# Performance work log

Hardware: AMD Instinct MI355X
Metric: run time of the kernel (lower is better)

## Reference

```python
import jax, jax.numpy as jnp
import numpy as np

NUM_EXPERTS = 8
TOP_K = 2
HIDDEN = 1024
INTER_TOTAL = 8192  # intermediate_size * experts_per_rank
B, S = 2, 2048


def setup_inputs() -> dict:
    key = jax.random.key(0)
    k1, k2, k3, k4, k5, k6 = jax.random.split(key, 6)
    T = B * S
    x = jax.random.normal(k1, (B, S, HIDDEN), dtype=jnp.float32)
    scores = jax.random.uniform(k2, (T, NUM_EXPERTS), dtype=jnp.float32)
    expert_weights = jax.random.uniform(k3, (T, TOP_K), dtype=jnp.float32)
    top_experts = jax.random.randint(k4, (T, TOP_K), 0, NUM_EXPERTS, dtype=jnp.int32)
    w1 = jax.random.normal(k5, (HIDDEN, INTER_TOTAL), dtype=jnp.float32) * 0.02
    w2 = jax.random.normal(k6, (INTER_TOTAL, HIDDEN), dtype=jnp.float32) * 0.02
    return {"x": x, "scores": scores, "expert_weights": expert_weights,
            "top_experts": top_experts, "w1": w1, "w2": w2}


def reference(x, scores, expert_weights, top_experts, w1, w2):
    # forward_once with expert_parallel_size == 1 (dropless MoE dispatch/combine).
    in_shape = x.shape
    T = in_shape[0] * in_shape[1]
    H = in_shape[-1]
    x_flat = x.reshape(T, H)

    flat_experts = top_experts.reshape(-1)          # [T*top_k]
    flat_weights = expert_weights.reshape(-1)       # [T*top_k]

    # ops.sort: stable radix sort of routed copies by expert id
    order = jnp.argsort(flat_experts, stable=True)  # "indices"
    token_idx = order // TOP_K                      # source token per sorted slot

    # padded_gather: bucket tokens per expert (padding rows are zeros and
    # pass through the bias-free MLP as zeros, so they never affect output)
    xg = x_flat[token_idx]                          # [T*top_k, H]

    # MLP: w1 -> gelu(tanh approx) -> w2
    h = jax.nn.gelu(xg @ w1, approximate=True)      # [T*top_k, inter*E]
    y = h @ w2                                      # [T*top_k, H]

    # padded_scatter: weighted combine back to token order
    w_sorted = flat_weights[order]
    out = jnp.zeros((T, H), dtype=x.dtype).at[token_idx].add(w_sorted[:, None] * y)
    return out.reshape(in_shape)
```

## Files before the change

### kernel.cpp

```cpp
#include <hip/hip_runtime.h>
#include <hip/hip_bf16.h>
#include <math.h>

#define HID 1024
#define INTER 8192
#define TT 4096

typedef __bf16 bf16x8 __attribute__((ext_vector_type(8)));
typedef float f32x4 __attribute__((ext_vector_type(4)));

__device__ __forceinline__ void gll16(const void* g, void* l) {
    __builtin_amdgcn_global_load_lds(
        (const __attribute__((address_space(1))) void*)g,
        (__attribute__((address_space(3))) void*)l, 16, 0, 0);
}

template <int OFF>
__device__ __forceinline__ bf16x8 ds_read128o(unsigned addr) {
    bf16x8 r;
    asm volatile("ds_read_b128 %0, %1 offset:%c2" : "=v"(r) : "v"(addr), "i"(OFF));
    return r;
}

__global__ void k_prep(const float* __restrict__ x, const float* __restrict__ ew,
                       __hip_bfloat16* __restrict__ xb, float* __restrict__ s,
                       int n4, int T) {
    int stride = gridDim.x * blockDim.x;
    for (int i = blockIdx.x * blockDim.x + threadIdx.x; i < n4; i += stride) {
        float4 v = ((const float4*)x)[i];
        __hip_bfloat16* o = xb + (size_t)i * 4;
        o[0] = __float2bfloat16(v.x);
        o[1] = __float2bfloat16(v.y);
        o[2] = __float2bfloat16(v.z);
        o[3] = __float2bfloat16(v.w);
    }
    for (int t = blockIdx.x * blockDim.x + threadIdx.x; t < T; t += stride)
        s[t] = ew[2 * t] + ew[2 * t + 1];
}

__global__ void k_tcast(const float* __restrict__ in, __hip_bfloat16* __restrict__ out,
                        int R, int C) {
    __shared__ float tile[32][33];
    const int tx = threadIdx.x & 31, ty = threadIdx.x >> 5;
    const int br = blockIdx.y * 32, bc = blockIdx.x * 32;
#pragma unroll
    for (int j = 0; j < 32; j += 8)
        tile[ty + j][tx] = in[(size_t)(br + ty + j) * C + bc + tx];
    __syncthreads();
#pragma unroll
    for (int j = 0; j < 32; j += 8)
        out[(size_t)(bc + ty + j) * R + br + tx] = __float2bfloat16(tile[tx][ty + j]);
}

template <int EPI>
__global__ __launch_bounds__(256, 2) void k_g128(
    const __hip_bfloat16* __restrict__ A, const __hip_bfloat16* __restrict__ Bt,
    __hip_bfloat16* __restrict__ hOut, float* __restrict__ fOut,
    const float* __restrict__ s, int Kfull, int nt, int Nout) {
    __shared__ __hip_bfloat16 sA[2][128][64];
    __shared__ __hip_bfloat16 sB[2][128][64];
    const int tid = threadIdx.x;
    const int lane = tid & 63, wid = tid >> 6;
    const int wr = wid >> 1, wc = wid & 1;

    const int nwg = gridDim.x * gridDim.y;
    const int wg = blockIdx.y * gridDim.x + blockIdx.x;
    const int swz = (wg & 7) * (nwg >> 3) + (wg >> 3);
    const int brow = (swz / gridDim.x) * 128;
    const int bcol = (swz % gridDim.x) * 128;
    const size_t kbase = (size_t)blockIdx.z * ((size_t)nt * 64);

    const int colsw = (((lane & 7) ^ (lane >> 3)) << 3);
    const __hip_bfloat16* gA2 =
        A + (size_t)(brow + wid * 32 + (lane >> 3)) * Kfull + kbase + colsw;
    const __hip_bfloat16* gB2 =
        Bt + (size_t)(bcol + wid * 32 + (lane >> 3)) * Kfull + kbase + colsw;
    char* ldsA2 = (char*)&sA[0][0][0] + wid * 4096;
    char* ldsB2 = (char*)&sB[0][0][0] + wid * 4096;
    const size_t chunkStep = (size_t)8 * Kfull;

    const unsigned baseA = (unsigned)(uintptr_t)&sA[0][0][0];
    const unsigned baseB = (unsigned)(uintptr_t)&sB[0][0][0];
    const unsigned g0 = (((lane >> 4)) ^ (lane & 7)) << 4;
    const unsigned g1 = ((4 + (lane >> 4)) ^ (lane & 7)) << 4;
    const unsigned rdA0 = baseA + wr * 8192 + (lane & 15) * 128 + g0;
    const unsigned rdA1 = baseA + wr * 8192 + (lane & 15) * 128 + g1;
    const unsigned rdB0 = baseB + wc * 8192 + (lane & 15) * 128 + g0;
    const unsigned rdB1 = baseB + wc * 8192 + (lane & 15) * 128 + g1;

    f32x4 acc[4][4] = {};
    bf16x8 aF[4][2], b01[2][2], b23[2][2];

#define STAGE_AB(bufoff, t)                                                    \
    do {                                                                       \
        _Pragma("unroll") for (int j = 0; j < 4; ++j)                          \
            gll16(gA2 + (size_t)j * chunkStep + (size_t)(t) * 64,              \
                  ldsA2 + (bufoff) + j * 1024);                                \
        _Pragma("unroll") for (int j = 0; j < 4; ++j)                          \
            gll16(gB2 + (size_t)j * chunkStep + (size_t)(t) * 64,              \
                  ldsB2 + (bufoff) + j * 1024);                                \
    } while (0)
#define PIN() __builtin_amdgcn_sched_barrier(0)
#define BAR()                              \
    do {                                   \
        PIN();                             \
        __builtin_amdgcn_s_barrier();      \
        PIN();                             \
    } while (0)
#define WAIT_LG4() __builtin_amdgcn_s_waitcnt(0xC47F)
#define WAIT_LG0() __builtin_amdgcn_s_waitcnt(0xC07F)
#define WAIT_VM0() __builtin_amdgcn_s_waitcnt(0x0F70)

    STAGE_AB(0u, 0);
    WAIT_VM0();
    BAR();

#pragma unroll 1
    for (int i = 0; i < nt; ++i) {
        const unsigned co = (i & 1) ? 16384u : 0u;
        const unsigned no = co ^ 16384u;
        const bool full = (i + 1 < nt);
        const unsigned aA0 = rdA0 + co, aA1 = rdA1 + co;
        const unsigned aB0 = rdB0 + co, aB1 = rdB1 + co;

        aF[0][0] = ds_read128o<0>(aA0);
        aF[0][1] = ds_read128o<0>(aA1);
        aF[1][0] = ds_read128o<2048>(aA0);
        aF[1][1] = ds_read128o<2048>(aA1);
        aF[2][0] = ds_read128o<4096>(aA0);
        aF[2][1] = ds_read128o<4096>(aA1);
        aF[3][0] = ds_read128o<6144>(aA0);
        aF[3][1] = ds_read128o<6144>(aA1);
        b01[0][0] = ds_read128o<0>(aB0);
        b01[0][1] = ds_read128o<0>(aB1);
        b01[1][0] = ds_read128o<2048>(aB0);
        b01[1][1] = ds_read128o<2048>(aB1);
        b23[0][0] = ds_read128o<4096>(aB0);
        b23[0][1] = ds_read128o<4096>(aB1);
        b23[1][0] = ds_read128o<6144>(aB0);
        b23[1][1] = ds_read128o<6144>(aB1);

        if (full) STAGE_AB(no, i + 1);

        __builtin_amdgcn_s_setprio(1);
        WAIT_LG4();
        PIN();
#pragma unroll
        for (int ks = 0; ks < 2; ++ks)
#pragma unroll
            for (int m = 0; m < 4; ++m)
#pragma unroll
                for (int n = 0; n < 2; ++n)
                    acc[m][n] = __builtin_amdgcn_mfma_f32_16x16x32_bf16(
                        aF[m][ks], b01[n][ks], acc[m][n], 0, 0, 0);
        PIN();
        WAIT_LG0();
        PIN();
#pragma unroll
        for (int ks = 0; ks < 2; ++ks)
#pragma unroll
            for (int m = 0; m < 4; ++m)
#pragma unroll
                for (int n = 0; n < 2; ++n)
                    acc[m][2 + n] = __builtin_amdgcn_mfma_f32_16x16x32_bf16(
                        aF[m][ks], b23[n][ks], acc[m][2 + n], 0, 0, 0);
        __builtin_amdgcn_s_setprio(0);
        PIN();
        WAIT_VM0();
        BAR();
    }

    const int orow = brow + wr * 64 + ((lane >> 4) << 2);
    const int ocol = bcol + wc * 64 + (lane & 15);
#pragma unroll
    for (int m = 0; m < 4; ++m) {
#pragma unroll
        for (int j = 0; j < 4; ++j) {
            const int r = orow + m * 16 + j;
            const size_t ro = (size_t)r * Nout;
            if (EPI == 0) {
#pragma unroll
                for (int n = 0; n < 4; ++n) {
                    float v = acc[m][n][j];
                    float u = 1.5957691216057308f * (v + 0.044715f * v * v * v);
                    float g = v / (1.0f + __expf(-u));
                    hOut[ro + ocol + n * 16] = __float2bfloat16(g);
                }
            } else {
                const float sc = s[r];
#pragma unroll
                for (int n = 0; n < 4; ++n)
                    unsafeAtomicAdd(&fOut[ro + ocol + n * 16], sc * acc[m][n][j]);
            }
        }
    }
#undef STAGE_AB
#undef PIN
#undef BAR
#undef WAIT_LG4
#undef WAIT_LG0
#undef WAIT_VM0
}

extern "C" void kernel_launch(void* const* d_in, const int* in_sizes, int n_in,
                              void* d_out, int out_size, void* d_ws, size_t ws_size,
                              hipStream_t stream) {
    const float* x = (const float*)d_in[0];
    const float* ew = (const float*)d_in[2];
    const float* w1 = (const float*)d_in[4];
    const float* w2 = (const float*)d_in[5];
    float* out = (float*)d_out;

    char* ws = (char*)d_ws;
    float* s = (float*)ws;
    __hip_bfloat16* xb = (__hip_bfloat16*)(ws + 16384);
    __hip_bfloat16* w1t = (__hip_bfloat16*)(ws + 16384 + 8388608);
    __hip_bfloat16* w2t = (__hip_bfloat16*)(ws + 16384 + 8388608 + 16777216);
    __hip_bfloat16* h = (__hip_bfloat16*)(ws + 16384 + 8388608 + 2 * 16777216);

    k_prep<<<1024, 256, 0, stream>>>(x, ew, xb, s, (TT * HID) / 4, TT);

    dim3 t1(INTER / 32, HID / 32);
    k_tcast<<<t1, 256, 0, stream>>>(w1, w1t, HID, INTER);
    dim3 t2(HID / 32, INTER / 32);
    k_tcast<<<t2, 256, 0, stream>>>(w2, w2t, INTER, HID);

    dim3 g1(INTER / 128, TT / 128, 1);
    k_g128<0><<<g1, 256, 0, stream>>>(xb, w1t, h, nullptr, nullptr, HID, HID / 64, INTER);

    hipMemsetAsync(out, 0, (size_t)TT * HID * sizeof(float), stream);
    dim3 g2(HID / 128, TT / 128, 4);
    k_g128<1><<<g2, 256, 0, stream>>>(h, w2t, nullptr, out, s, INTER, 2048 / 64, HID);
}
```

Baseline: 226.4 us.

## Switch GEMM to triple-buffered K=32 tiles with two-stage prefetch

Both GEMMs now use a K-tile of 32 instead of 64 and three LDS buffers instead of two. Loads are issued two iterations ahead, and each iteration waits only for the older tile. LDS use drops from 64KB to 48KB, and launch bounds rise to 3 blocks per CU to allow more occupancy. The cost is twice as many barriers per K step and half as many MFMAs per barrier, and the new swizzle and pointer layout must still be correct.

```diff
diff --git a/kernel.cpp b/kernel.cpp
--- a/kernel.cpp
+++ b/kernel.cpp
@@ -53,12 +53,12 @@
 }
 
 template <int EPI>
-__global__ __launch_bounds__(256, 2) void k_g128(
+__global__ __launch_bounds__(256, 3) void k_g3(
     const __hip_bfloat16* __restrict__ A, const __hip_bfloat16* __restrict__ Bt,
     __hip_bfloat16* __restrict__ hOut, float* __restrict__ fOut,
     const float* __restrict__ s, int Kfull, int nt, int Nout) {
-    __shared__ __hip_bfloat16 sA[2][128][64];
-    __shared__ __hip_bfloat16 sB[2][128][64];
+    __shared__ __hip_bfloat16 sA[3][128][32];
+    __shared__ __hip_bfloat16 sB[3][128][32];
     const int tid = threadIdx.x;
     const int lane = tid & 63, wid = tid >> 6;
     const int wr = wid >> 1, wc = wid & 1;
@@ -68,37 +68,32 @@
     const int swz = (wg & 7) * (nwg >> 3) + (wg >> 3);
     const int brow = (swz / gridDim.x) * 128;
     const int bcol = (swz % gridDim.x) * 128;
-    const size_t kbase = (size_t)blockIdx.z * ((size_t)nt * 64);
-
-    const int colsw = (((lane & 7) ^ (lane >> 3)) << 3);
+    const size_t kbase = (size_t)blockIdx.z * ((size_t)nt * 32);
+
+    const int colsw = (((lane & 3) ^ ((lane >> 2) & 3)) << 3);
     const __hip_bfloat16* gA2 =
-        A + (size_t)(brow + wid * 32 + (lane >> 3)) * Kfull + kbase + colsw;
+        A + (size_t)(brow + wid * 32 + (lane >> 2)) * Kfull + kbase + colsw;
     const __hip_bfloat16* gB2 =
-        Bt + (size_t)(bcol + wid * 32 + (lane >> 3)) * Kfull + kbase + colsw;
-    char* ldsA2 = (char*)&sA[0][0][0] + wid * 4096;
-    char* ldsB2 = (char*)&sB[0][0][0] + wid * 4096;
-    const size_t chunkStep = (size_t)8 * Kfull;
+        Bt + (size_t)(bcol + wid * 32 + (lane >> 2)) * Kfull + kbase + colsw;
+    char* ldsA2 = (char*)&sA[0][0][0] + wid * 2048;
+    char* ldsB2 = (char*)&sB[0][0][0] + wid * 2048;
+    const size_t chunkStep = (size_t)16 * Kfull;
 
     const unsigned baseA = (unsigned)(uintptr_t)&sA[0][0][0];
     const unsigned baseB = (unsigned)(uintptr_t)&sB[0][0][0];
-    const unsigned g0 = (((lane >> 4)) ^ (lane & 7)) << 4;
-    const unsigned g1 = ((4 + (lane >> 4)) ^ (lane & 7)) << 4;
-    const unsigned rdA0 = baseA + wr * 8192 + (lane & 15) * 128 + g0;
-    const unsigned rdA1 = baseA + wr * 8192 + (lane & 15) * 128 + g1;
-    const unsigned rdB0 = baseB + wc * 8192 + (lane & 15) * 128 + g0;
-    const unsigned rdB1 = baseB + wc * 8192 + (lane & 15) * 128 + g1;
+    const unsigned gsw = (((lane >> 4) ^ (lane & 3)) << 4);
+    const unsigned rdA = baseA + wr * 4096 + (lane & 15) * 64 + gsw;
+    const unsigned rdB = baseB + wc * 4096 + (lane & 15) * 64 + gsw;
 
     f32x4 acc[4][4] = {};
-    bf16x8 aF[4][2], b01[2][2], b23[2][2];
-
-#define STAGE_AB(bufoff, t)                                                    \
+    bf16x8 aF[4], bF[4];
+
+#define STAGE(bufoff, t)                                                       \
     do {                                                                       \
-        _Pragma("unroll") for (int j = 0; j < 4; ++j)                          \
-            gll16(gA2 + (size_t)j * chunkStep + (size_t)(t) * 64,              \
-                  ldsA2 + (bufoff) + j * 1024);                                \
-        _Pragma("unroll") for (int j = 0; j < 4; ++j)                          \
-            gll16(gB2 + (size_t)j * chunkStep + (size_t)(t) * 64,              \
-                  ldsB2 + (bufoff) + j * 1024);                                \
+        gll16(gA2 + (size_t)(t) * 32, ldsA2 + (bufoff));                       \
+        gll16(gA2 + chunkStep + (size_t)(t) * 32, ldsA2 + (bufoff) + 1024);    \
+        gll16(gB2 + (size_t)(t) * 32, ldsB2 + (bufoff));                       \
+        gll16(gB2 + chunkStep + (size_t)(t) * 32, ldsB2 + (bufoff) + 1024);    \
     } while (0)
 #define PIN() __builtin_amdgcn_sched_barrier(0)
 #define BAR()                              \
@@ -107,67 +102,62 @@
         __builtin_amdgcn_s_barrier();      \
         PIN();                             \
     } while (0)
-#define WAIT_LG4() __builtin_amdgcn_s_waitcnt(0xC47F)
+#define WAIT_LG2() __builtin_amdgcn_s_waitcnt(0xC27F)
 #define WAIT_LG0() __builtin_amdgcn_s_waitcnt(0xC07F)
+#define WAIT_VM4() __builtin_amdgcn_s_waitcnt(0x0F74)
 #define WAIT_VM0() __builtin_amdgcn_s_waitcnt(0x0F70)
 
-    STAGE_AB(0u, 0);
-    WAIT_VM0();
+    STAGE(0u, 0);
+    STAGE(8192u, 1);
+    WAIT_VM4();
     BAR();
 
+    unsigned co = 0u, c1 = 8192u, c2 = 16384u;
 #pragma unroll 1
     for (int i = 0; i < nt; ++i) {
-        const unsigned co = (i & 1) ? 16384u : 0u;
-        const unsigned no = co ^ 16384u;
-        const bool full = (i + 1 < nt);
-        const unsigned aA0 = rdA0 + co, aA1 = rdA1 + co;
-        const unsigned aB0 = rdB0 + co, aB1 = rdB1 + co;
-
-        aF[0][0] = ds_read128o<0>(aA0);
-        aF[0][1] = ds_read128o<0>(aA1);
-        aF[1][0] = ds_read128o<2048>(aA0);
-        aF[1][1] = ds_read128o<2048>(aA1);
-        aF[2][0] = ds_read128o<4096>(aA0);
-        aF[2][1] = ds_read128o<4096>(aA1);
-        aF[3][0] = ds_read128o<6144>(aA0);
-        aF[3][1] = ds_read128o<6144>(aA1);
-        b01[0][0] = ds_read128o<0>(aB0);
-        b01[0][1] = ds_read128o<0>(aB1);
-        b01[1][0] = ds_read128o<2048>(aB0);
-        b01[1][1] = ds_read128o<2048>(aB1);
-        b23[0][0] = ds_read128o<4096>(aB0);
-        b23[0][1] = ds_read128o<4096>(aB1);
-        b23[1][0] = ds_read128o<6144>(aB0);
-        b23[1][1] = ds_read128o<6144>(aB1);
-
-        if (full) STAGE_AB(no, i + 1);
+        const bool more = (i + 2 < nt);
+        const unsigned aA = rdA + co, aB = rdB + co;
+
+        aF[0] = ds_read128o<0>(aA);
+        aF[1] = ds_read128o<1024>(aA);
+        aF[2] = ds_read128o<2048>(aA);
+        aF[3] = ds_read128o<3072>(aA);
+        bF[0] = ds_read128o<0>(aB);
+        bF[1] = ds_read128o<1024>(aB);
+        bF[2] = ds_read128o<2048>(aB);
+        bF[3] = ds_read128o<3072>(aB);
+
+        if (more) STAGE(c2, i + 2);
 
         __builtin_amdgcn_s_setprio(1);
-        WAIT_LG4();
-        PIN();
-#pragma unroll
-        for (int ks = 0; ks < 2; ++ks)
-#pragma unroll
-            for (int m = 0; m < 4; ++m)
-#pragma unroll
-                for (int n = 0; n < 2; ++n)
-                    acc[m][n] = __builtin_amdgcn_mfma_f32_16x16x32_bf16(
-                        aF[m][ks], b01[n][ks], acc[m][n], 0, 0, 0);
+        WAIT_LG2();
+        PIN();
+#pragma unroll
+        for (int m = 0; m < 4; ++m)
+#pragma unroll
+            for (int n = 0; n < 2; ++n)
+                acc[m][n] = __builtin_amdgcn_mfma_f32_16x16x32_bf16(
+                    aF[m], bF[n], acc[m][n], 0, 0, 0);
         PIN();
         WAIT_LG0();
         PIN();
 #pragma unroll
-        for (int ks = 0; ks < 2; ++ks)
-#pragma unroll
-            for (int m = 0; m < 4; ++m)
-#pragma unroll
-                for (int n = 0; n < 2; ++n)
-                    acc[m][2 + n] = __builtin_amdgcn_mfma_f32_16x16x32_bf16(
-                        aF[m][ks], b23[n][ks], acc[m][2 + n], 0, 0, 0);
+        for (int m = 0; m < 4; ++m)
+#pragma unroll
+            for (int n = 0; n < 2; ++n)
+                acc[m][2 + n] = __builtin_amdgcn_mfma_f32_16x16x32_bf16(
+                    aF[m], bF[2 + n], acc[m][2 + n], 0, 0, 0);
         __builtin_amdgcn_s_setprio(0);
         PIN();
-        WAIT_VM0();
+        if (more)
+            WAIT_VM4();
+        else
+            WAIT_VM0();
         BAR();
+        const unsigned t = co;
+        co = c1;
+        c1 = c2;
+        c2 = t;
     }
 
     const int orow = brow + wr * 64 + ((lane >> 4) << 2);
@@ -194,11 +184,12 @@
             }
         }
     }
-#undef STAGE_AB
+#undef STAGE
 #undef PIN
 #undef BAR
-#undef WAIT_LG4
+#undef WAIT_LG2
 #undef WAIT_LG0
+#undef WAIT_VM4
 #undef WAIT_VM0
 }
 
@@ -226,9 +217,9 @@
     k_tcast<<<t2, 256, 0, stream>>>(w2, w2t, INTER, HID);
 
     dim3 g1(INTER / 128, TT / 128, 1);
-    k_g128<0><<<g1, 256, 0, stream>>>(xb, w1t, h, nullptr, nullptr, HID, HID / 64, INTER);
+    k_g3<0><<<g1, 256, 0, stream>>>(xb, w1t, h, nullptr, nullptr, HID, HID / 32, INTER);
 
     hipMemsetAsync(out, 0, (size_t)TT * HID * sizeof(float), stream);
     dim3 g2(HID / 128, TT / 128, 4);
-    k_g128<1><<<g2, 256, 0, stream>>>(h, w2t, nullptr, out, s, INTER, 2048 / 64, HID);
-}
+    k_g3<1><<<g2, 256, 0, stream>>>(h, w2t, nullptr, out, s, INTER, 2048 / 32, HID);
+}
```

After: 232.7 us. +2.8%, slower.

## Prefetch next LDS fragments into registers and merge prep kernels into one launch

Applied to the files above, without the earlier changes.

The GEMM main loop now double-buffers register fragments: the next tile's LDS reads and the global-to-LDS stage two tiles ahead are issued before the current tile's MFMAs, with the loop unrolled by two to swap register sets. This is meant to hide LDS read latency behind matrix math instead of waiting on it each iteration. The input cast and the two weight transpose-casts are merged into a single kernel launch to cut launch overhead. It roughly doubles fragment register use, which risks spills under the two-waves launch bound. The unroll-by-two loop assumes an even tile count.

```diff
diff --git a/kernel.cpp b/kernel.cpp
--- a/kernel.cpp
+++ b/kernel.cpp
@@ -22,27 +22,12 @@
     return r;
 }
 
-__global__ void k_prep(const float* __restrict__ x, const float* __restrict__ ew,
-                       __hip_bfloat16* __restrict__ xb, float* __restrict__ s,
-                       int n4, int T) {
-    int stride = gridDim.x * blockDim.x;
-    for (int i = blockIdx.x * blockDim.x + threadIdx.x; i < n4; i += stride) {
-        float4 v = ((const float4*)x)[i];
-        __hip_bfloat16* o = xb + (size_t)i * 4;
-        o[0] = __float2bfloat16(v.x);
-        o[1] = __float2bfloat16(v.y);
-        o[2] = __float2bfloat16(v.z);
-        o[3] = __float2bfloat16(v.w);
-    }
-    for (int t = blockIdx.x * blockDim.x + threadIdx.x; t < T; t += stride)
-        s[t] = ew[2 * t] + ew[2 * t + 1];
-}
-
-__global__ void k_tcast(const float* __restrict__ in, __hip_bfloat16* __restrict__ out,
-                        int R, int C) {
+__device__ __forceinline__ void tcast_tile(const float* __restrict__ in,
+                                           __hip_bfloat16* __restrict__ out,
+                                           int R, int C, int bx, int by, int tid) {
     __shared__ float tile[32][33];
-    const int tx = threadIdx.x & 31, ty = threadIdx.x >> 5;
-    const int br = blockIdx.y * 32, bc = blockIdx.x * 32;
+    const int tx = tid & 31, ty = tid >> 5;
+    const int br = by * 32, bc = bx * 32;
 #pragma unroll
     for (int j = 0; j < 32; j += 8)
         tile[ty + j][tx] = in[(size_t)(br + ty + j) * C + bc + tx];
@@ -52,8 +37,35 @@
         out[(size_t)(bc + ty + j) * R + br + tx] = __float2bfloat16(tile[tx][ty + j]);
 }
 
+__global__ void k_prep(const float* __restrict__ x, const float* __restrict__ ew,
+                       const float* __restrict__ w1, const float* __restrict__ w2,
+                       __hip_bfloat16* __restrict__ xb, float* __restrict__ s,
+                       __hip_bfloat16* __restrict__ w1t, __hip_bfloat16* __restrict__ w2t) {
+    const int bid = blockIdx.x, tid = threadIdx.x;
+    if (bid < 1024) {
+        const int n4 = (TT * HID) / 4;
+        const int stride = 1024 * 256;
+        for (int i = bid * 256 + tid; i < n4; i += stride) {
+            float4 v = ((const float4*)x)[i];
+            __hip_bfloat16* o = xb + (size_t)i * 4;
+            o[0] = __float2bfloat16(v.x);
+            o[1] = __float2bfloat16(v.y);
+            o[2] = __float2bfloat16(v.z);
+            o[3] = __float2bfloat16(v.w);
+        }
+        for (int t = bid * 256 + tid; t < TT; t += stride)
+            s[t] = ew[2 * t] + ew[2 * t + 1];
+    } else if (bid < 1024 + 8192) {
+        const int b = bid - 1024;
+        tcast_tile(w1, w1t, HID, INTER, b % 256, b / 256, tid);
+    } else {
+        const int b = bid - (1024 + 8192);
+        tcast_tile(w2, w2t, INTER, HID, b % 32, b / 32, tid);
+    }
+}
+
 template <int EPI>
-__global__ __launch_bounds__(256, 2) void k_g128(
+__global__ __launch_bounds__(256, 2) void k_gpf(
     const __hip_bfloat16* __restrict__ A, const __hip_bfloat16* __restrict__ Bt,
     __hip_bfloat16* __restrict__ hOut, float* __restrict__ fOut,
     const float* __restrict__ s, int Kfull, int nt, int Nout) {
@@ -89,7 +101,7 @@
     const unsigned rdB1 = baseB + wc * 8192 + (lane & 15) * 128 + g1;
 
     f32x4 acc[4][4] = {};
-    bf16x8 aF[4][2], b01[2][2], b23[2][2];
+    bf16x8 aC[4][2], bC[4][2], aN[4][2], bN[4][2];
 
 #define STAGE_AB(bufoff, t)                                                    \
     do {                                                                       \
@@ -107,67 +119,60 @@
         __builtin_amdgcn_s_barrier();      \
         PIN();                             \
     } while (0)
-#define WAIT_LG4() __builtin_amdgcn_s_waitcnt(0xC47F)
 #define WAIT_LG0() __builtin_amdgcn_s_waitcnt(0xC07F)
 #define WAIT_VM0() __builtin_amdgcn_s_waitcnt(0x0F70)
+
+#define READS(AN, BN, off)                         \
+    do {                                           \
+        AN[0][0] = ds_read128o<0>(rdA0 + (off));   \
+        AN[0][1] = ds_read128o<0>(rdA1 + (off));   \
+        AN[1][0] = ds_read128o<2048>(rdA0 + (off)); \
+        AN[1][1] = ds_read128o<2048>(rdA1 + (off)); \
+        AN[2][0] = ds_read128o<4096>(rdA0 + (off)); \
+        AN[2][1] = ds_read128o<4096>(rdA1 + (off)); \
+        AN[3][0] = ds_read128o<6144>(rdA0 + (off)); \
+        AN[3][1] = ds_read128o<6144>(rdA1 + (off)); \
+        BN[0][0] = ds_read128o<0>(rdB0 + (off));   \
+        BN[0][1] = ds_read128o<0>(rdB1 + (off));   \
+        BN[1][0] = ds_read128o<2048>(rdB0 + (off)); \
+        BN[1][1] = ds_read128o<2048>(rdB1 + (off)); \
+        BN[2][0] = ds_read128o<4096>(rdB0 + (off)); \
+        BN[2][1] = ds_read128o<4096>(rdB1 + (off)); \
+        BN[3][0] = ds_read128o<6144>(rdB0 + (off)); \
+        BN[3][1] = ds_read128o<6144>(rdB1 + (off)); \
+    } while (0)
+
+#define BODY(AC, BC, AN, BN, i, co, no)                                        \
+    do {                                                                       \
+        if ((i) + 1 < nt) READS(AN, BN, no);                                   \
+        if ((i) + 2 < nt) STAGE_AB(co, (i) + 2);                               \
+        PIN();                                                                 \
+        __builtin_amdgcn_s_setprio(1);                                         \
+        _Pragma("unroll") for (int ks = 0; ks < 2; ++ks)                       \
+        _Pragma("unroll") for (int m = 0; m < 4; ++m)                          \
+        _Pragma("unroll") for (int n = 0; n < 4; ++n)                          \
+            acc[m][n] = __builtin_amdgcn_mfma_f32_16x16x32_bf16(               \
+                AC[m][ks], BC[n][ks], acc[m][n], 0, 0, 0);                     \
+        __builtin_amdgcn_s_setprio(0);                                         \
+        PIN();                                                                 \
+        WAIT_LG0();                                                            \
+        WAIT_VM0();                                                            \
+        BAR();                                                                 \
+    } while (0)
 
     STAGE_AB(0u, 0);
     WAIT_VM0();
     BAR();
+    READS(aC, bC, 0u);
+    if (1 < nt) STAGE_AB(16384u, 1);
+    WAIT_LG0();
+    WAIT_VM0();
+    BAR();
 
 #pragma unroll 1
-    for (int i = 0; i < nt; ++i) {
-        const unsigned co = (i & 1) ? 16384u : 0u;
-        const unsigned no = co ^ 16384u;
-        const bool full = (i + 1 < nt);
-        const unsigned aA0 = rdA0 + co, aA1 = rdA1 + co;
-        const unsigned aB0 = rdB0 + co, aB1 = rdB1 + co;
-
-        aF[0][0] = ds_read128o<0>(aA0);
-        aF[0][1] = ds_read128o<0>(aA1);
-        aF[1][0] = ds_read128o<2048>(aA0);
-        aF[1][1] = ds_read128o<2048>(aA1);
-        aF[2][0] = ds_read128o<4096>(aA0);
-        aF[2][1] = ds_read128o<4096>(aA1);
-        aF[3][0] = ds_read128o<6144>(aA0);
-        aF[3][1] = ds_read128o<6144>(aA1);
-        b01[0][0] = ds_read128o<0>(aB0);
-        b01[0][1] = ds_read128o<0>(aB1);
-        b01[1][0] = ds_read128o<2048>(aB0);
-        b01[1][1] = ds_read128o<2048>(aB1);
-        b23[0][0] = ds_read128o<4096>(aB0);
-        b23[0][1] = ds_read128o<4096>(aB1);
-        b23[1][0] = ds_read128o<6144>(aB0);
-        b23[1][1] = ds_read128o<6144>(aB1);
-
-        if (full) STAGE_AB(no, i + 1);
-
-        __builtin_amdgcn_s_setprio(1);
-        WAIT_LG4();
-        PIN();
-#pragma unroll
-        for (int ks = 0; ks < 2; ++ks)
-#pragma unroll
-            for (int m = 0; m < 4; ++m)
-#pragma unroll
-                for (int n = 0; n < 2; ++n)
-                    acc[m][n] = __builtin_amdgcn_mfma_f32_16x16x32_bf16(
-                        aF[m][ks], b01[n][ks], acc[m][n], 0, 0, 0);
-        PIN();
-        WAIT_LG0();
-        PIN();
-#pragma unroll
-        for (int ks = 0; ks < 2; ++ks)
-#pragma unroll
-            for (int m = 0; m < 4; ++m)
-#pragma unroll
-                for (int n = 0; n < 2; ++n)
-                    acc[m][2 + n] = __builtin_amdgcn_mfma_f32_16x16x32_bf16(
-                        aF[m][ks], b23[n][ks], acc[m][2 + n], 0, 0, 0);
-        __builtin_amdgcn_s_setprio(0);
-        PIN();
-        WAIT_VM0();
-        BAR();
+    for (int i = 0; i < nt; i += 2) {
+        BODY(aC, bC, aN, bN, i, 0u, 16384u);
+        BODY(aN, bN, aC, bC, i + 1, 16384u, 0u);
     }
 
     const int orow = brow + wr * 64 + ((lane >> 4) << 2);
@@ -197,9 +202,10 @@
 #undef STAGE_AB
 #undef PIN
 #undef BAR
-#undef WAIT_LG4
 #undef WAIT_LG0
 #undef WAIT_VM0
+#undef READS
+#undef BODY
 }
 
 extern "C" void kernel_launch(void* const* d_in, const int* in_sizes, int n_in,
@@ -218,17 +224,12 @@
     __hip_bfloat16* w2t = (__hip_bfloat16*)(ws + 16384 + 8388608 + 16777216);
     __hip_bfloat16* h = (__hip_bfloat16*)(ws + 16384 + 8388608 + 2 * 16777216);
 
-    k_prep<<<1024, 256, 0, stream>>>(x, ew, xb, s, (TT * HID) / 4, TT);
-
-    dim3 t1(INTER / 32, HID / 32);
-    k_tcast<<<t1, 256, 0, stream>>>(w1, w1t, HID, INTER);
-    dim3 t2(HID / 32, INTER / 32);
-    k_tcast<<<t2, 256, 0, stream>>>(w2, w2t, INTER, HID);
+    k_prep<<<1024 + 8192 + 8192, 256, 0, stream>>>(x, ew, w1, w2, xb, s, w1t, w2t);
 
     dim3 g1(INTER / 128, TT / 128, 1);
-    k_g128<0><<<g1, 256, 0, stream>>>(xb, w1t, h, nullptr, nullptr, HID, HID / 64, INTER);
+    k_gpf<0><<<g1, 256, 0, stream>>>(xb, w1t, h, nullptr, nullptr, HID, HID / 64, INTER);
 
     hipMemsetAsync(out, 0, (size_t)TT * HID * sizeof(float), stream);
     dim3 g2(HID / 128, TT / 128, 4);
-    k_g128<1><<<g2, 256, 0, stream>>>(h, w2t, nullptr, out, s, INTER, 2048 / 64, HID);
-}
+    k_gpf<1><<<g2, 256, 0, stream>>>(h, w2t, nullptr, out, s, INTER, 2048 / 64, HID);
+}
```

New measurement: 221.9 us. 1.02x faster.
